# Kernel tuning notes

Hardware: AMD Instinct MI355X
Metric: run time of the kernel (lower is better)

The kernel has to match this reference:

```python
import jax, jax.numpy as jnp
import numpy as np


def setup_inputs() -> dict:
    key = jax.random.key(0)
    ks = jax.random.split(key, 6)
    B, C, H, W = 8, 128, 48, 64
    return {
        "feature0": jax.random.normal(ks[0], (B, C, H, W), dtype=jnp.float32),
        "feature1": jax.random.normal(ks[1], (B, C, H, W), dtype=jnp.float32),
        "q_w": jax.random.normal(ks[2], (C, C), dtype=jnp.float32) * 0.05,
        "q_b": jax.random.normal(ks[3], (C,), dtype=jnp.float32) * 0.05,
        "k_w": jax.random.normal(ks[4], (C, C), dtype=jnp.float32) * 0.05,
        "k_b": jax.random.normal(ks[5], (C,), dtype=jnp.float32) * 0.05,
        "scale_idx": 0,
    }


def reference(feature0, feature1, q_w, q_b, k_w, k_b, scale_idx):
    # scale_idx=0 -> corr_radius=-1 (global correlation), prop_radius=-1 (global self-attn)
    b, c, h, w = feature0.shape
    n = h * w
    inv_sqrt_c = 1.0 / jnp.sqrt(jnp.asarray(c, feature0.dtype))

    f0 = feature0.reshape(b, c, n).transpose(0, 2, 1)  # [B, N, C]
    f1 = feature1.reshape(b, c, n)                     # [B, C, N]

    corr = jnp.einsum('bnc,bcm->bnm', f0, f1) * inv_sqrt_c  # [B, N, N]
    prob = jax.nn.softmax(corr, axis=-1)
    ys, xs = jnp.meshgrid(jnp.arange(h, dtype=feature0.dtype),
                          jnp.arange(w, dtype=feature0.dtype), indexing='ij')
    grid = jnp.stack([xs, ys], axis=-1).reshape(n, 2)        # [N, 2] (x, y)
    correspondence = jnp.einsum('bnm,md->bnd', prob, grid)   # [B, N, 2]
    flow_pred = (correspondence - grid[None]).reshape(b, h, w, 2).transpose(0, 3, 1, 2)  # [B,2,H,W]

    # ---- SelfAttnPropagation (global): q = q_proj(f0), k = k_proj(q) ----
    q = f0 @ q_w.T + q_b              # [B, N, C]
    k = q @ k_w.T + k_b               # [B, N, C]  (projected from q, per unimatch)
    scores = jnp.einsum('bnc,bmc->bnm', q, k) * inv_sqrt_c
    attn = jax.nn.softmax(scores, axis=-1)
    v = jax.lax.stop_gradient(flow_pred).reshape(b, 2, n).transpose(0, 2, 1)  # [B, N, 2]
    flow = jnp.einsum('bnm,bmd->bnd', attn, v).reshape(b, h, w, 2).transpose(0, 3, 1, 2)

    return flow, flow_pred
```

## Files before the change

### kernel.cpp

```cpp
#include <hip/hip_runtime.h>

constexpr int BATCH = 8;
constexpr int CH    = 128;
constexpr int NPix  = 3072;
constexpr int NT    = 48;
constexpr int NCHUNK = 4;
constexpr int TPC   = NT / NCHUNK;
constexpr int MPC   = TPC * 64;
constexpr int TILE_SHORTS = 64 * CH;
constexpr float INV_SQRT_C = 0.08838834764831845f;

typedef __bf16 bf16x8 __attribute__((ext_vector_type(8)));
typedef float  floatx4 __attribute__((ext_vector_type(4)));

static __device__ __forceinline__ unsigned short f2bf(float f) {
  unsigned int u = __float_as_uint(f);
  u += 0x7fff + ((u >> 16) & 1);
  return (unsigned short)(u >> 16);
}
static __device__ __forceinline__ float bf2f(unsigned short h) {
  return __uint_as_float((unsigned int)h << 16);
}

static __device__ __forceinline__ void loadT(float (*T)[65],
                                             const float* __restrict__ src, int t) {
  const int cc = 4 * (t & 15);
  const int kb = t >> 4;
#pragma unroll
  for (int p = 0; p < 8; ++p) {
    const int k = kb + 16 * p;
    const float4 v = *(const float4*)(src + (size_t)k * NPix + cc);
    T[k][cc] = v.x; T[k][cc + 1] = v.y; T[k][cc + 2] = v.z; T[k][cc + 3] = v.w;
  }
}

static __device__ __forceinline__ void stageK(unsigned short* __restrict__ dst,
                                              const unsigned short* __restrict__ src,
                                              int t) {
#pragma unroll
  for (int i = 0; i < 4; ++i)
    *(uint4*)&dst[(i * 256 + t) * 8] = *(const uint4*)(src + (size_t)(i * 256 + t) * 8);
}

__global__ __launch_bounds__(256) void setup_kernel(
    const float* __restrict__ qw, const float* __restrict__ qb,
    const float* __restrict__ kw, const float* __restrict__ kb,
    unsigned short* __restrict__ qwb_hi, unsigned short* __restrict__ qwb_lo,
    unsigned short* __restrict__ w2b_hi, unsigned short* __restrict__ w2b_lo,
    float* __restrict__ b2) {
  __shared__ float W2s[16][CH];
  const int t = threadIdx.x;
  const bool second = blockIdx.x >= 8;
  const int B = blockIdx.x & 7;
  if (second) {
#pragma unroll
    for (int p = 0; p < 8; ++p) {
      const int idx = p * 256 + t;
      const int r = idx >> 7, i = idx & 127;
      const int o = B * 16 + r;
      float acc = 0.f;
#pragma unroll 8
      for (int j = 0; j < CH; ++j)
        acc = fmaf(kw[o * CH + j], qw[j * CH + i], acc);
      W2s[r][i] = acc;
    }
    if (t < 16) {
      const int o = B * 16 + t;
      float a2 = kb[o];
#pragma unroll 8
      for (int j = 0; j < CH; ++j) a2 = fmaf(kw[o * CH + j], qb[j], a2);
      b2[o] = a2;
    }
    __syncthreads();
  }
  const int cidx = B * 256 + t;
  const int l2 = cidx & 63, kc = (cidx >> 6) & 3;
  const int co = B * 16 + (l2 & 15);
  const int ci0 = kc * 32 + (l2 >> 4) * 8;
  unsigned short vh[8], vl[8];
#pragma unroll
  for (int j = 0; j < 8; ++j) {
    const float v = second ? W2s[l2 & 15][ci0 + j] : qw[co * CH + ci0 + j];
    const unsigned short h = f2bf(v);
    vh[j] = h;
    vl[j] = f2bf(v - bf2f(h));
  }
  *(uint4*)((second ? w2b_hi : qwb_hi) + (size_t)cidx * 8) = *(uint4*)vh;
  *(uint4*)((second ? w2b_lo : qwb_lo) + (size_t)cidx * 8) = *(uint4*)vl;
}

__global__ __launch_bounds__(256, 3) void preproc_kernel(
    const float* __restrict__ f0, const float* __restrict__ f1,
    const float* __restrict__ qb, const float* __restrict__ b2,
    const unsigned short* __restrict__ qwb_hi, const unsigned short* __restrict__ qwb_lo,
    const unsigned short* __restrict__ w2b_hi, const unsigned short* __restrict__ w2b_lo,
    unsigned short* __restrict__ f0t, unsigned short* __restrict__ f1t,
    unsigned short* __restrict__ qt, unsigned short* __restrict__ kt) {
  __shared__ float T[CH][65];
  const int t = threadIdx.x;
  const bool isF0 = blockIdx.x >= BATCH * NT;
  const int bi = blockIdx.x - (isF0 ? BATCH * NT : 0);
  const int b = bi / NT, tile = bi % NT;
  const size_t tb = (size_t)bi * TILE_SHORTS;

  loadT(T, (isF0 ? f0 : f1) + (size_t)b * CH * NPix + tile * 64, t);
  __syncthreads();

  unsigned short* gdst = (isF0 ? f0t : f1t) + tb;
#pragma unroll
  for (int i = 0; i < 4; ++i) {
    const int oi   = i * 256 + t;
    const int lane2 = oi & 63;
    const int kc   = (oi >> 6) & 3;
    const int c    = oi >> 8;
    const int r    = c * 16 + (lane2 & 15);
    const int ch0  = kc * 32 + (lane2 >> 4) * 8;
    unsigned short v[8];
#pragma unroll
    for (int j = 0; j < 8; ++j) v[j] = f2bf(T[ch0 + j][r]);
    *(uint4*)(gdst + (size_t)oi * 8) = *(uint4*)v;
  }
  if (!isF0) return;

  const int lane = t & 63, wave = t >> 6, quad = lane >> 4, lrow = lane & 15;

  bf16x8 ah[4], al[4];
#pragma unroll
  for (int kc = 0; kc < 4; ++kc) {
    unsigned short vh[8], vl[8];
#pragma unroll
    for (int j = 0; j < 8; ++j) {
      const float v = T[kc * 32 + quad * 8 + j][wave * 16 + lrow];
      const unsigned short h = f2bf(v);
      vh[j] = h;
      vl[j] = f2bf(v - bf2f(h));
    }
    ah[kc] = *(bf16x8*)vh;
    al[kc] = *(bf16x8*)vl;
  }

#pragma unroll
  for (int mat = 0; mat < 2; ++mat) {
    const unsigned short* wh = mat ? w2b_hi : qwb_hi;
    const unsigned short* wl = mat ? w2b_lo : qwb_lo;
    const float* bias = mat ? b2 : qb;
    unsigned short* dst = (mat ? kt : qt) + tb;
#pragma unroll
    for (int cb = 0; cb < 8; ++cb) {
      floatx4 acc = {0.f, 0.f, 0.f, 0.f};
#pragma unroll
      for (int kc = 0; kc < 4; ++kc) {
        const bf16x8 bh = *(const bf16x8*)(wh + ((cb * 4 + kc) * 64 + lane) * 8);
        const bf16x8 bl = *(const bf16x8*)(wl + ((cb * 4 + kc) * 64 + lane) * 8);
        acc = __builtin_amdgcn_mfma_f32_16x16x32_bf16(ah[kc], bh, acc, 0, 0, 0);
        acc = __builtin_amdgcn_mfma_f32_16x16x32_bf16(al[kc], bh, acc, 0, 0, 0);
        acc = __builtin_amdgcn_mfma_f32_16x16x32_bf16(ah[kc], bl, acc, 0, 0, 0);
      }
      const int co = cb * 16 + lrow;
      const float bv = bias[co];
      const int kcq = co >> 5, l2hi = ((co >> 3) & 3) * 16, j = co & 7;
#pragma unroll
      for (int r = 0; r < 4; ++r) {
        const int rl = quad * 4 + r;
        dst[((wave * 4 + kcq) * 64 + l2hi + rl) * 8 + j] = f2bf(acc[r] + bv);
      }
    }
  }
}

__global__ __launch_bounds__(256, 3) void corr_part_kernel(
    const unsigned short* __restrict__ f0t, const unsigned short* __restrict__ f1t,
    float* __restrict__ P) {
  __shared__ unsigned short Ks[2][TILE_SHORTS];
  const int t = threadIdx.x;
  const int b = blockIdx.x / ((NT / 2) * NCHUNK);
  const int rem = blockIdx.x % ((NT / 2) * NCHUNK);
  const int tp = rem >> 2, chunk = rem & 3;
  const int lane = t & 63, wave = t >> 6, quad = lane >> 4, lrow = lane & 15;

  bf16x8 af[2][4];
#pragma unroll
  for (int s = 0; s < 2; ++s) {
    const unsigned short* qp = f0t + (size_t)(b * NT + 2 * tp + s) * TILE_SHORTS;
#pragma unroll
    for (int kc = 0; kc < 4; ++kc)
      af[s][kc] = *(const bf16x8*)(qp + ((wave * 4 + kc) * 64 + lane) * 8);
  }

  float l[2][4] = {{0}}, sx[2][4] = {{0}}, sy[2][4] = {{0}};

  stageK(Ks[0], f1t + (size_t)(b * NT + chunk * TPC) * TILE_SHORTS, t);

  for (int mi = 0; mi < TPC; ++mi) {
    const int mt = chunk * TPC + mi;
    __syncthreads();
    if (mi + 1 < TPC)
      stageK(Ks[(mi + 1) & 1],
             f1t + (size_t)(b * NT + mt + 1) * TILE_SHORTS, t);
    const unsigned short* KB = Ks[mi & 1];

    float ts[2][4] = {{0}};
#pragma unroll
    for (int c = 0; c < 4; ++c) {
      const float x = (float)(c * 16 + lrow);
      bf16x8 bfr[4];
#pragma unroll
      for (int kc = 0; kc < 4; ++kc)
        bfr[kc] = *(const bf16x8*)&KB[((c * 4 + kc) * 64 + lane) * 8];
#pragma unroll
      for (int s = 0; s < 2; ++s) {
        floatx4 acc = {0.f, 0.f, 0.f, 0.f};
#pragma unroll
        for (int kc = 0; kc < 4; ++kc)
          acc = __builtin_amdgcn_mfma_f32_16x16x32_bf16(af[s][kc], bfr[kc], acc, 0, 0, 0);
#pragma unroll
        for (int r = 0; r < 4; ++r) {
          const float e = __expf(acc[r] * INV_SQRT_C);
          ts[s][r] += e;
          sx[s][r] = fmaf(e, x, sx[s][r]);
        }
      }
    }
    const float y = (float)mt;
#pragma unroll
    for (int s = 0; s < 2; ++s)
#pragma unroll
      for (int r = 0; r < 4; ++r) {
        l[s][r] += ts[s][r];
        sy[s][r] = fmaf(y, ts[s][r], sy[s][r]);
      }
  }

#pragma unroll
  for (int off = 1; off < 16; off <<= 1)
#pragma unroll
    for (int s = 0; s < 2; ++s)
#pragma unroll
      for (int r = 0; r < 4; ++r) {
        l[s][r] += __shfl_xor(l[s][r], off);
        sx[s][r] += __shfl_xor(sx[s][r], off);
        sy[s][r] += __shfl_xor(sy[s][r], off);
      }
  if (lrow == 0) {
#pragma unroll
    for (int s = 0; s < 2; ++s)
#pragma unroll
      for (int r = 0; r < 4; ++r) {
        const int g = (b * NT + 2 * tp + s) * 64 + wave * 16 + quad * 4 + r;
        P[(g * 3 + 0) * 4 + chunk] = l[s][r];
        P[(g * 3 + 1) * 4 + chunk] = sx[s][r];
        P[(g * 3 + 2) * 4 + chunk] = sy[s][r];
      }
  }
}

__global__ __launch_bounds__(256, 3) void attn_part_kernel(
    const unsigned short* __restrict__ qt, const unsigned short* __restrict__ kt,
    const float* __restrict__ P, float* __restrict__ flow_pred,
    float* __restrict__ P2) {
  __shared__ unsigned short Ks[2][TILE_SHORTS];
  __shared__ float FP[MPC][2];
  const int t = threadIdx.x;
  const int b = blockIdx.x / ((NT / 2) * NCHUNK);
  const int rem = blockIdx.x % ((NT / 2) * NCHUNK);
  const int tp = rem >> 2, chunk = rem & 3;
  const int lane = t & 63, wave = t >> 6, quad = lane >> 4, lrow = lane & 15;

  for (int rr = t; rr < MPC; rr += 256) {
    const int n = chunk * MPC + rr;
    const int g = b * NPix + n;
    const float4 lv = *(const float4*)&P[(g * 3 + 0) * 4];
    const float4 xv = *(const float4*)&P[(g * 3 + 1) * 4];
    const float4 yv = *(const float4*)&P[(g * 3 + 2) * 4];
    const float lsum = (lv.x + lv.y) + (lv.z + lv.w);
    const float inv = 1.f / lsum;
    FP[rr][0] = ((xv.x + xv.y) + (xv.z + xv.w)) * inv - (float)(n & 63);
    FP[rr][1] = ((yv.x + yv.y) + (yv.z + yv.w)) * inv - (float)(n >> 6);
  }

  if (tp == 0) {
    __syncthreads();
    for (int rr = t; rr < MPC; rr += 256) {
      const int n = chunk * MPC + rr;
      flow_pred[(size_t)(b * 2 + 0) * NPix + n] = FP[rr][0];
      flow_pred[(size_t)(b * 2 + 1) * NPix + n] = FP[rr][1];
    }
  }

  bf16x8 af[2][4];
#pragma unroll
  for (int s = 0; s < 2; ++s) {
    const unsigned short* qp = qt + (size_t)(b * NT + 2 * tp + s) * TILE_SHORTS;
#pragma unroll
    for (int kc = 0; kc < 4; ++kc)
      af[s][kc] = *(const bf16x8*)(qp + ((wave * 4 + kc) * 64 + lane) * 8);
  }

  float l[2][4] = {{0}}, sx[2][4] = {{0}}, sy[2][4] = {{0}};

  stageK(Ks[0], kt + (size_t)(b * NT + chunk * TPC) * TILE_SHORTS, t);

  for (int mi = 0; mi < TPC; ++mi) {
    const int mt = chunk * TPC + mi;
    __syncthreads();
    if (mi + 1 < TPC)
      stageK(Ks[(mi + 1) & 1],
             kt + (size_t)(b * NT + mt + 1) * TILE_SHORTS, t);
    const unsigned short* KB = Ks[mi & 1];

#pragma unroll
    for (int c = 0; c < 4; ++c) {
      const int mloc = mi * 64 + c * 16 + lrow;
      const float vx = FP[mloc][0], vy = FP[mloc][1];
      bf16x8 bfr[4];
#pragma unroll
      for (int kc = 0; kc < 4; ++kc)
        bfr[kc] = *(const bf16x8*)&KB[((c * 4 + kc) * 64 + lane) * 8];
#pragma unroll
      for (int s = 0; s < 2; ++s) {
        floatx4 acc = {0.f, 0.f, 0.f, 0.f};
#pragma unroll
        for (int kc = 0; kc < 4; ++kc)
          acc = __builtin_amdgcn_mfma_f32_16x16x32_bf16(af[s][kc], bfr[kc], acc, 0, 0, 0);
#pragma unroll
        for (int r = 0; r < 4; ++r) {
          const float e = __expf(acc[r] * INV_SQRT_C);
          l[s][r] += e;
          sx[s][r] = fmaf(e, vx, sx[s][r]);
          sy[s][r] = fmaf(e, vy, sy[s][r]);
        }
      }
    }
  }

#pragma unroll
  for (int off = 1; off < 16; off <<= 1)
#pragma unroll
    for (int s = 0; s < 2; ++s)
#pragma unroll
      for (int r = 0; r < 4; ++r) {
        l[s][r] += __shfl_xor(l[s][r], off);
        sx[s][r] += __shfl_xor(sx[s][r], off);
        sy[s][r] += __shfl_xor(sy[s][r], off);
      }
  if (lrow == 0) {
#pragma unroll
    for (int s = 0; s < 2; ++s)
#pragma unroll
      for (int r = 0; r < 4; ++r) {
        const int g = (b * NT + 2 * tp + s) * 64 + wave * 16 + quad * 4 + r;
        P2[(g * 3 + 0) * 4 + chunk] = l[s][r];
        P2[(g * 3 + 1) * 4 + chunk] = sx[s][r];
        P2[(g * 3 + 2) * 4 + chunk] = sy[s][r];
      }
  }
}

__global__ __launch_bounds__(256) void reduce_attn_kernel(
    const float* __restrict__ P2, float* __restrict__ flow) {
  const int g = blockIdx.x * 256 + threadIdx.x;
  const float4 lv = *(const float4*)&P2[(g * 3 + 0) * 4];
  const float4 xv = *(const float4*)&P2[(g * 3 + 1) * 4];
  const float4 yv = *(const float4*)&P2[(g * 3 + 2) * 4];
  const float l = (lv.x + lv.y) + (lv.z + lv.w);
  const float inv = 1.f / l;
  const int b = g / NPix, n = g % NPix;
  flow[(size_t)(b * 2 + 0) * NPix + n] = ((xv.x + xv.y) + (xv.z + xv.w)) * inv;
  flow[(size_t)(b * 2 + 1) * NPix + n] = ((yv.x + yv.y) + (yv.z + yv.w)) * inv;
}

extern "C" void kernel_launch(void* const* d_in, const int* in_sizes, int n_in,
                              void* d_out, int out_size, void* d_ws,
                              size_t ws_size, hipStream_t stream) {
  const float* f0  = (const float*)d_in[0];
  const float* f1  = (const float*)d_in[1];
  const float* q_w = (const float*)d_in[2];
  const float* q_b = (const float*)d_in[3];
  const float* k_w = (const float*)d_in[4];
  const float* k_b = (const float*)d_in[5];

  float* out       = (float*)d_out;
  float* flow      = out;
  float* flow_pred = out + (size_t)BATCH * 2 * NPix;

  const size_t tile_elems = (size_t)BATCH * NT * TILE_SHORTS;
  unsigned short* f0t = (unsigned short*)d_ws;
  unsigned short* f1t = f0t + tile_elems;
  unsigned short* qt  = f1t + tile_elems;
  unsigned short* kt  = qt + tile_elems;
  unsigned short* qwb_hi = kt + tile_elems;
  unsigned short* qwb_lo = qwb_hi + 2048 * 8;
  unsigned short* w2b_hi = qwb_lo + 2048 * 8;
  unsigned short* w2b_lo = w2b_hi + 2048 * 8;
  float* b2 = (float*)(w2b_lo + 2048 * 8);
  float* P  = b2 + CH;
  float* P2 = P + (size_t)BATCH * NPix * 12;

  setup_kernel<<<16, 256, 0, stream>>>(q_w, q_b, k_w, k_b,
                                       qwb_hi, qwb_lo, w2b_hi, w2b_lo, b2);
  preproc_kernel<<<2 * BATCH * NT, 256, 0, stream>>>(
      f0, f1, q_b, b2, qwb_hi, qwb_lo, w2b_hi, w2b_lo, f0t, f1t, qt, kt);
  corr_part_kernel<<<BATCH * (NT / 2) * NCHUNK, 256, 0, stream>>>(f0t, f1t, P);
  attn_part_kernel<<<BATCH * (NT / 2) * NCHUNK, 256, 0, stream>>>(qt, kt, P,
                                                                  flow_pred, P2);
  reduce_attn_kernel<<<96, 256, 0, stream>>>(P2, flow);
}
```

Measured before the change: 187.1 us.

## Fuse final reductions into partial kernels via last-block atomic counters

Adds per-tile atomic counters so the last chunk block of each tile pair sums the partials and writes flow_pred or flow, which removes the separate reduce kernel and the flow_pred write-out inside attn_part. Also replaces __expf with exp2f using a prescaled constant, and loads B fragments inside the MFMA loop instead of staging them up front. In exchange it adds a hipMemsetAsync, threadfences and atomics, and the tail of each tile's work is serialized onto one block.

```diff
diff --git a/kernel.cpp b/kernel.cpp
--- a/kernel.cpp
+++ b/kernel.cpp
@@ -9,6 +9,7 @@
 constexpr int MPC   = TPC * 64;
 constexpr int TILE_SHORTS = 64 * CH;
 constexpr float INV_SQRT_C = 0.08838834764831845f;
+constexpr float SC_EXP2 = 0.08838834764831845f * 1.4426950408889634f;
 
 typedef __bf16 bf16x8 __attribute__((ext_vector_type(8)));
 typedef float  floatx4 __attribute__((ext_vector_type(4)));
@@ -170,8 +171,10 @@
 
 __global__ __launch_bounds__(256, 3) void corr_part_kernel(
     const unsigned short* __restrict__ f0t, const unsigned short* __restrict__ f1t,
-    float* __restrict__ P) {
+    float* __restrict__ P, float* __restrict__ flow_pred,
+    unsigned int* __restrict__ ctr) {
   __shared__ unsigned short Ks[2][TILE_SHORTS];
+  __shared__ int isLast;
   const int t = threadIdx.x;
   const int b = blockIdx.x / ((NT / 2) * NCHUNK);
   const int rem = blockIdx.x % ((NT / 2) * NCHUNK);
@@ -203,19 +206,17 @@
 #pragma unroll
     for (int c = 0; c < 4; ++c) {
       const float x = (float)(c * 16 + lrow);
-      bf16x8 bfr[4];
-#pragma unroll
-      for (int kc = 0; kc < 4; ++kc)
-        bfr[kc] = *(const bf16x8*)&KB[((c * 4 + kc) * 64 + lane) * 8];
 #pragma unroll
       for (int s = 0; s < 2; ++s) {
         floatx4 acc = {0.f, 0.f, 0.f, 0.f};
 #pragma unroll
-        for (int kc = 0; kc < 4; ++kc)
-          acc = __builtin_amdgcn_mfma_f32_16x16x32_bf16(af[s][kc], bfr[kc], acc, 0, 0, 0);
+        for (int kc = 0; kc < 4; ++kc) {
+          const bf16x8 bf = *(const bf16x8*)&KB[((c * 4 + kc) * 64 + lane) * 8];
+          acc = __builtin_amdgcn_mfma_f32_16x16x32_bf16(af[s][kc], bf, acc, 0, 0, 0);
+        }
 #pragma unroll
         for (int r = 0; r < 4; ++r) {
-          const float e = __expf(acc[r] * INV_SQRT_C);
+          const float e = exp2f(acc[r] * SC_EXP2);
           ts[s][r] += e;
           sx[s][r] = fmaf(e, x, sx[s][r]);
         }
@@ -252,14 +253,38 @@
         P[(g * 3 + 2) * 4 + chunk] = sy[s][r];
       }
   }
+
+  __syncthreads();
+  if (t == 0) {
+    __threadfence();
+    isLast = (atomicAdd(&ctr[b * (NT / 2) + tp], 1u) == NCHUNK - 1);
+  }
+  __syncthreads();
+  if (isLast) {
+    __threadfence();
+    if (t < 128) {
+      const int n = (2 * tp + (t >> 6)) * 64 + (t & 63);
+      const int g = b * NPix + n;
+      const float4 lv = *(const float4*)&P[(g * 3 + 0) * 4];
+      const float4 xv = *(const float4*)&P[(g * 3 + 1) * 4];
+      const float4 yv = *(const float4*)&P[(g * 3 + 2) * 4];
+      const float lsum = (lv.x + lv.y) + (lv.z + lv.w);
+      const float inv = 1.f / lsum;
+      flow_pred[(size_t)(b * 2 + 0) * NPix + n] =
+          ((xv.x + xv.y) + (xv.z + xv.w)) * inv - (float)(n & 63);
+      flow_pred[(size_t)(b * 2 + 1) * NPix + n] =
+          ((yv.x + yv.y) + (yv.z + yv.w)) * inv - (float)(n >> 6);
+    }
+  }
 }
 
 __global__ __launch_bounds__(256, 3) void attn_part_kernel(
     const unsigned short* __restrict__ qt, const unsigned short* __restrict__ kt,
-    const float* __restrict__ P, float* __restrict__ flow_pred,
-    float* __restrict__ P2) {
+    const float* __restrict__ P, float* __restrict__ P2,
+    float* __restrict__ flow, unsigned int* __restrict__ ctr) {
   __shared__ unsigned short Ks[2][TILE_SHORTS];
   __shared__ float FP[MPC][2];
+  __shared__ int isLast;
   const int t = threadIdx.x;
   const int b = blockIdx.x / ((NT / 2) * NCHUNK);
   const int rem = blockIdx.x % ((NT / 2) * NCHUNK);
@@ -278,15 +303,6 @@
     FP[rr][1] = ((yv.x + yv.y) + (yv.z + yv.w)) * inv - (float)(n >> 6);
   }
 
-  if (tp == 0) {
-    __syncthreads();
-    for (int rr = t; rr < MPC; rr += 256) {
-      const int n = chunk * MPC + rr;
-      flow_pred[(size_t)(b * 2 + 0) * NPix + n] = FP[rr][0];
-      flow_pred[(size_t)(b * 2 + 1) * NPix + n] = FP[rr][1];
-    }
-  }
-
   bf16x8 af[2][4];
 #pragma unroll
   for (int s = 0; s < 2; ++s) {
@@ -312,19 +328,17 @@
     for (int c = 0; c < 4; ++c) {
       const int mloc = mi * 64 + c * 16 + lrow;
       const float vx = FP[mloc][0], vy = FP[mloc][1];
-      bf16x8 bfr[4];
-#pragma unroll
-      for (int kc = 0; kc < 4; ++kc)
-        bfr[kc] = *(const bf16x8*)&KB[((c * 4 + kc) * 64 + lane) * 8];
 #pragma unroll
       for (int s = 0; s < 2; ++s) {
         floatx4 acc = {0.f, 0.f, 0.f, 0.f};
 #pragma unroll
-        for (int kc = 0; kc < 4; ++kc)
-          acc = __builtin_amdgcn_mfma_f32_16x16x32_bf16(af[s][kc], bfr[kc], acc, 0, 0, 0);
+        for (int kc = 0; kc < 4; ++kc) {
+          const bf16x8 bf = *(const bf16x8*)&KB[((c * 4 + kc) * 64 + lane) * 8];
+          acc = __builtin_amdgcn_mfma_f32_16x16x32_bf16(af[s][kc], bf, acc, 0, 0, 0);
+        }
 #pragma unroll
         for (int r = 0; r < 4; ++r) {
-          const float e = __expf(acc[r] * INV_SQRT_C);
+          const float e = exp2f(acc[r] * SC_EXP2);
           l[s][r] += e;
           sx[s][r] = fmaf(e, vx, sx[s][r]);
           sy[s][r] = fmaf(e, vy, sy[s][r]);
@@ -354,19 +368,27 @@
         P2[(g * 3 + 2) * 4 + chunk] = sy[s][r];
       }
   }
-}
-
-__global__ __launch_bounds__(256) void reduce_attn_kernel(
-    const float* __restrict__ P2, float* __restrict__ flow) {
-  const int g = blockIdx.x * 256 + threadIdx.x;
-  const float4 lv = *(const float4*)&P2[(g * 3 + 0) * 4];
-  const float4 xv = *(const float4*)&P2[(g * 3 + 1) * 4];
-  const float4 yv = *(const float4*)&P2[(g * 3 + 2) * 4];
-  const float l = (lv.x + lv.y) + (lv.z + lv.w);
-  const float inv = 1.f / l;
-  const int b = g / NPix, n = g % NPix;
-  flow[(size_t)(b * 2 + 0) * NPix + n] = ((xv.x + xv.y) + (xv.z + xv.w)) * inv;
-  flow[(size_t)(b * 2 + 1) * NPix + n] = ((yv.x + yv.y) + (yv.z + yv.w)) * inv;
+
+  __syncthreads();
+  if (t == 0) {
+    __threadfence();
+    isLast = (atomicAdd(&ctr[b * (NT / 2) + tp], 1u) == NCHUNK - 1);
+  }
+  __syncthreads();
+  if (isLast) {
+    __threadfence();
+    if (t < 128) {
+      const int n = (2 * tp + (t >> 6)) * 64 + (t & 63);
+      const int g = b * NPix + n;
+      const float4 lv = *(const float4*)&P2[(g * 3 + 0) * 4];
+      const float4 xv = *(const float4*)&P2[(g * 3 + 1) * 4];
+      const float4 yv = *(const float4*)&P2[(g * 3 + 2) * 4];
+      const float lsum = (lv.x + lv.y) + (lv.z + lv.w);
+      const float inv = 1.f / lsum;
+      flow[(size_t)(b * 2 + 0) * NPix + n] = ((xv.x + xv.y) + (xv.z + xv.w)) * inv;
+      flow[(size_t)(b * 2 + 1) * NPix + n] = ((yv.x + yv.y) + (yv.z + yv.w)) * inv;
+    }
+  }
 }
 
 extern "C" void kernel_launch(void* const* d_in, const int* in_sizes, int n_in,
@@ -395,13 +417,15 @@
   float* b2 = (float*)(w2b_lo + 2048 * 8);
   float* P  = b2 + CH;
   float* P2 = P + (size_t)BATCH * NPix * 12;
+  unsigned int* ctr = (unsigned int*)(P2 + (size_t)BATCH * NPix * 12);
+  hipMemsetAsync(ctr, 0, 2 * BATCH * (NT / 2) * sizeof(unsigned int), stream);
 
   setup_kernel<<<16, 256, 0, stream>>>(q_w, q_b, k_w, k_b,
                                        qwb_hi, qwb_lo, w2b_hi, w2b_lo, b2);
   preproc_kernel<<<2 * BATCH * NT, 256, 0, stream>>>(
       f0, f1, q_b, b2, qwb_hi, qwb_lo, w2b_hi, w2b_lo, f0t, f1t, qt, kt);
-  corr_part_kernel<<<BATCH * (NT / 2) * NCHUNK, 256, 0, stream>>>(f0t, f1t, P);
-  attn_part_kernel<<<BATCH * (NT / 2) * NCHUNK, 256, 0, stream>>>(qt, kt, P,
-                                                                  flow_pred, P2);
-  reduce_attn_kernel<<<96, 256, 0, stream>>>(P2, flow);
-}
+  corr_part_kernel<<<BATCH * (NT / 2) * NCHUNK, 256, 0, stream>>>(
+      f0t, f1t, P, flow_pred, ctr);
+  attn_part_kernel<<<BATCH * (NT / 2) * NCHUNK, 256, 0, stream>>>(
+      qt, kt, P, P2, flow, ctr + BATCH * (NT / 2));
+}
```

New measurement: 318.6 us. 70.3% more time.
